# Kernel optimization log

Measured on AMD Instinct MI355X. Metric: run time of the kernel, lower is better.

The kernel has to match this reference:

```python
import jax, jax.numpy as jnp
import numpy as np

HEADS = 8
DIM_HEAD = 64
SCALE = DIM_HEAD ** -0.5
K = 7


def _conv(x, w, stride):
    return jax.lax.conv_general_dilated(
        x, w, window_strides=(stride, stride), padding='VALID',
        dimension_numbers=('NHWC', 'HWIO', 'NHWC'))


def _split_heads(t):
    # 'b x y (h d) -> (b h) (x y) d'
    b, X, Y, hd = t.shape
    d = hd // HEADS
    t = t.reshape(b, X, Y, HEADS, d)
    t = t.transpose(0, 3, 1, 2, 4)  # b h x y d
    return t.reshape(b * HEADS, X * Y, d)


def setup_inputs() -> dict:
    key = jax.random.key(0)
    ks = jax.random.split(key, 6)
    dim, inner = 256, HEADS * DIM_HEAD
    x = jax.random.normal(ks[0], (8, 84, 84, dim), dtype=jnp.float32)
    w_q = jax.random.normal(ks[1], (1, 1, dim, inner), dtype=jnp.float32) * 0.02
    w_kv = jax.random.normal(ks[2], (K, K, dim, 2 * inner), dtype=jnp.float32) * 0.02
    w_out = jax.random.normal(ks[3], (1, 1, inner, dim), dtype=jnp.float32) * 0.02
    b_out = jnp.zeros((dim,), dtype=jnp.float32)
    return {"x": x, "w_q": w_q, "w_kv": w_kv, "w_out": w_out, "b_out": b_out}


def reference(x, w_q, w_kv, w_out, b_out):
    b, X, Y, _ = x.shape
    q = _conv(x, w_q, 1)          # [b, X, Y, inner]
    kv = _conv(x, w_kv, K)        # [b, X/k, Y/k, 2*inner]
    k, v = jnp.split(kv, 2, axis=-1)
    q = _split_heads(q)           # [(b h), XY, d]
    k = _split_heads(k)           # [(b h), xy, d]
    v = _split_heads(v)
    dots = jnp.einsum('bid,bjd->bij', q, k) * SCALE
    attn = jax.nn.softmax(dots, axis=-1)
    out = jnp.einsum('bij,bjd->bid', attn, v)  # [(b h), XY, d]
    out = out.reshape(b, HEADS, X, Y, DIM_HEAD).transpose(0, 2, 3, 1, 4)
    out = out.reshape(b, X, Y, HEADS * DIM_HEAD)
    out = _conv(out, w_out, 1) + b_out  # dropout rate 0 -> identity
    return out
```

## Files before the change

### kernel.cpp

```cpp
#include <hip/hip_runtime.h>

typedef unsigned short u16;
typedef __bf16 bf16x8 __attribute__((ext_vector_type(8)));
typedef float f32x4 __attribute__((ext_vector_type(4)));

__device__ __forceinline__ u16 f2b(float f) {
    unsigned int u = __float_as_uint(f);
    u += 0x7fffu + ((u >> 16) & 1u);
    return (u16)(u >> 16);
}

__device__ __forceinline__ int xcd_chunk(int wg, int n) {
    int q = n >> 3, r = n & 7;
    int x = wg & 7, i = wg >> 3;
    return (x < r ? x * (q + 1) : r * (q + 1) + (x - r) * q) + i;
}

__global__ __launch_bounds__(256) void k_pack_x(const float* __restrict__ x,
                                                u16* __restrict__ xp) {
    int v = blockIdx.x * 256 + threadIdx.x;
    int c0 = (v & 31) << 3;
    int pix = v >> 5;
    int b = pix / 7056;
    int r = pix - b * 7056;
    int y = r / 84;
    int xx = r - y * 84;
    int opix = (b * 144 + (y / 7) * 12 + (xx / 7)) * 49 + (y % 7) * 7 + (xx % 7);
    const float4* src = reinterpret_cast<const float4*>(x + ((size_t)pix << 8) + c0);
    float4 f0 = src[0], f1 = src[1];
    uint4 o;
    o.x = (unsigned)f2b(f0.x) | ((unsigned)f2b(f0.y) << 16);
    o.y = (unsigned)f2b(f0.z) | ((unsigned)f2b(f0.w) << 16);
    o.z = (unsigned)f2b(f1.x) | ((unsigned)f2b(f1.y) << 16);
    o.w = (unsigned)f2b(f1.z) | ((unsigned)f2b(f1.w) << 16);
    *reinterpret_cast<uint4*>(xp + ((size_t)opix << 8) + c0) = o;
}

__global__ __launch_bounds__(256) void k_tconv(const float* __restrict__ in,
                                               u16* __restrict__ out, int R, int C,
                                               float scale) {
    __shared__ float tile[32][33];
    int c0 = blockIdx.x << 5, r0 = blockIdx.y << 5;
    int tx = threadIdx.x, ty = threadIdx.y;
#pragma unroll
    for (int i = 0; i < 4; i++)
        tile[ty + (i << 3)][tx] = in[(size_t)(r0 + ty + (i << 3)) * C + c0 + tx];
    __syncthreads();
#pragma unroll
    for (int i = 0; i < 4; i++)
        out[(size_t)(c0 + ty + (i << 3)) * R + r0 + tx] = f2b(tile[tx][ty + (i << 3)] * scale);
}

__global__ __launch_bounds__(256) void k_kvproj(const u16* __restrict__ xp,
                                                const u16* __restrict__ wkvT,
                                                float* __restrict__ parts) {
    __shared__ u16 As[128][72];
    __shared__ u16 Bs[128][72];
    const int lin = xcd_chunk(blockIdx.x, 504);
    const int mt = lin % 9;
    const int ntsp = lin / 9;
    const int nt = ntsp & 7;
    const int sp = ntsp >> 3;
    const int tid = threadIdx.x;
    const int wave = tid >> 6, lane = tid & 63;
    const int wr = wave >> 1, wc = wave & 1;
    const int lrow = lane & 15, lkg = lane >> 4;
    const u16* Ag = xp + (size_t)(mt * 128) * 12544 + sp * 1792;
    const u16* Bg = wkvT + (size_t)(nt * 128) * 12544 + sp * 1792;
    const int srow = tid >> 3, scol = (tid & 7) << 3;
    f32x4 acc[4][4];
#pragma unroll
    for (int m = 0; m < 4; m++)
#pragma unroll
        for (int n = 0; n < 4; n++)
#pragma unroll
            for (int i = 0; i < 4; i++) acc[m][n][i] = 0.f;

    for (int ks = 0; ks < 28; ks++) {
        const int k0 = ks * 64;
        __syncthreads();
#pragma unroll
        for (int p = 0; p < 4; p++) {
            int rr = srow + (p << 5);
            *reinterpret_cast<bf16x8*>(&As[rr][scol]) =
                *reinterpret_cast<const bf16x8*>(Ag + (size_t)rr * 12544 + k0 + scol);
            *reinterpret_cast<bf16x8*>(&Bs[rr][scol]) =
                *reinterpret_cast<const bf16x8*>(Bg + (size_t)rr * 12544 + k0 + scol);
        }
        __syncthreads();
#pragma unroll
        for (int kk = 0; kk < 2; kk++) {
            const int ko = (kk << 5) + (lkg << 3);
            bf16x8 a[4], bb[4];
#pragma unroll
            for (int m = 0; m < 4; m++)
                a[m] = *reinterpret_cast<const bf16x8*>(&As[(wr << 6) + (m << 4) + lrow][ko]);
#pragma unroll
            for (int n = 0; n < 4; n++)
                bb[n] = *reinterpret_cast<const bf16x8*>(&Bs[(wc << 6) + (n << 4) + lrow][ko]);
#pragma unroll
            for (int m = 0; m < 4; m++)
#pragma unroll
                for (int n = 0; n < 4; n++)
                    acc[m][n] = __builtin_amdgcn_mfma_f32_16x16x32_bf16(a[m], bb[n], acc[m][n], 0, 0, 0);
        }
    }
    float* outp = parts + (size_t)sp * 1179648;
#pragma unroll
    for (int m = 0; m < 4; m++)
#pragma unroll
        for (int n = 0; n < 4; n++)
#pragma unroll
            for (int i = 0; i < 4; i++) {
                int row = (mt << 7) + (wr << 6) + (m << 4) + (lkg << 2) + i;
                int col = (nt << 7) + (wc << 6) + (n << 4) + lrow;
                outp[(size_t)row * 1024 + col] = acc[m][n][i];
            }
}

__global__ __launch_bounds__(256) void k_kvfin(const float* __restrict__ parts,
                                               u16* __restrict__ Kf, u16* __restrict__ Vf) {
    int idx = blockIdx.x * 256 + threadIdx.x;
    int m = idx >> 10, n = idx & 1023;
    float s = 0.f;
#pragma unroll
    for (int sp = 0; sp < 7; sp++) s += parts[(size_t)sp * 1179648 + idx];
    int b = m / 144, pi = m - b * 144;
    int h = (n & 511) >> 6, d = n & 63;
    int bh = (b << 3) + h;
    if (n < 512) {
        int fc = pi >> 4, lr = pi & 15;
        int ks = d >> 5, lg = (d >> 3) & 3, e = d & 7;
        Kf[((((size_t)bh * 9 + fc) << 1) + ks) * 512 + (((lg << 4) + lr) << 3) + e] = f2b(s);
    } else {
        int nf = d >> 4, lr = d & 15;
        int ks = pi >> 5, lg = (pi >> 3) & 3, e = pi & 7;
        Vf[(((size_t)bh * 4 + nf) * 5 + ks) * 512 + (((lg << 4) + lr) << 3) + e] = f2b(s);
    }
}

__global__ __launch_bounds__(256) void k_qproj(const u16* __restrict__ xp,
                                               const u16* __restrict__ wqT,
                                               u16* __restrict__ Qf) {
    __shared__ u16 As[128][72];
    __shared__ u16 Bs[128][72];
    const int lin = xcd_chunk(blockIdx.x, 1764);
    const int nt = lin & 3, mt = lin >> 2;
    const int tid = threadIdx.x;
    const int wave = tid >> 6, lane = tid & 63;
    const int wr = wave >> 1, wc = wave & 1;
    const int lrow = lane & 15, lkg = lane >> 4;
    const u16* Ag = xp + (size_t)(mt * 128) * 256;
    const u16* Bg = wqT + (size_t)(nt * 128) * 256;
    const int srow = tid >> 3, scol = (tid & 7) << 3;
    f32x4 acc[4][4];
#pragma unroll
    for (int m = 0; m < 4; m++)
#pragma unroll
        for (int n = 0; n < 4; n++)
#pragma unroll
            for (int i = 0; i < 4; i++) acc[m][n][i] = 0.f;

    for (int ks = 0; ks < 4; ks++) {
        const int k0 = ks * 64;
        __syncthreads();
#pragma unroll
        for (int p = 0; p < 4; p++) {
            int rr = srow + (p << 5);
            *reinterpret_cast<bf16x8*>(&As[rr][scol]) =
                *reinterpret_cast<const bf16x8*>(Ag + (size_t)rr * 256 + k0 + scol);
            *reinterpret_cast<bf16x8*>(&Bs[rr][scol]) =
                *reinterpret_cast<const bf16x8*>(Bg + (size_t)rr * 256 + k0 + scol);
        }
        __syncthreads();
#pragma unroll
        for (int kk = 0; kk < 2; kk++) {
            const int ko = (kk << 5) + (lkg << 3);
            bf16x8 a[4], bb[4];
#pragma unroll
            for (int m = 0; m < 4; m++)
                a[m] = *reinterpret_cast<const bf16x8*>(&As[(wr << 6) + (m << 4) + lrow][ko]);
#pragma unroll
            for (int n = 0; n < 4; n++)
                bb[n] = *reinterpret_cast<const bf16x8*>(&Bs[(wc << 6) + (n << 4) + lrow][ko]);
#pragma unroll
            for (int m = 0; m < 4; m++)
#pragma unroll
                for (int n = 0; n < 4; n++)
                    acc[m][n] = __builtin_amdgcn_mfma_f32_16x16x32_bf16(a[m], bb[n], acc[m][n], 0, 0, 0);
        }
    }
#pragma unroll
    for (int m = 0; m < 4; m++)
#pragma unroll
        for (int n = 0; n < 4; n++)
#pragma unroll
            for (int i = 0; i < 4; i++) {
                int row = (mt << 7) + (wr << 6) + (m << 4) + (lkg << 2) + i;
                int col = (nt << 7) + (wc << 6) + (n << 4) + lrow;
                int b = row / 7056, pp = row - b * 7056;
                int h = col >> 6, d = col & 63;
                int bh = (b << 3) + h;
                int tt = pp >> 4, flr = pp & 15;
                int fks = d >> 5, flg = (d >> 3) & 3, fe = d & 7;
                Qf[((((size_t)bh * 441 + tt) << 1) + fks) * 512 + (((flg << 4) + flr) << 3) + fe] =
                    f2b(acc[m][n][i]);
            }
}

__global__ __launch_bounds__(128, 8) void k_attn(const u16* __restrict__ Qf,
                                                 const u16* __restrict__ Kf,
                                                 const u16* __restrict__ Vf,
                                                 u16* __restrict__ O) {
    __shared__ u16 smem[2 * 16 * 168];
    const int wv = threadIdx.x >> 6, lane = threadIdx.x & 63;
    const int t = blockIdx.x;
    const int h = (blockIdx.y << 1) + wv;
    const int b = blockIdx.z;
    const int lrow = lane & 15, lkg = lane >> 4;
    const int bh = (b << 3) + h;
    u16* sm = smem + wv * (16 * 168);
    const int l8 = lane << 3;

    const u16* Qg = Qf + ((((size_t)bh * 441 + t) << 1) << 9);
    const u16* Kg = Kf + (((size_t)bh * 9) << 10);
    const u16* Vg = Vf + ((size_t)bh * 20) * 512;

    f32x4 da[9];
#pragma unroll
    for (int fc = 0; fc < 9; fc++)
#pragma unroll
        for (int i = 0; i < 4; i++) da[fc][i] = 0.f;
#pragma unroll
    for (int ks = 0; ks < 2; ks++) {
        bf16x8 aq = *reinterpret_cast<const bf16x8*>(Qg + (ks << 9) + l8);
#pragma unroll
        for (int fc = 0; fc < 9; fc++) {
            bf16x8 bk = *reinterpret_cast<const bf16x8*>(Kg + ((((fc << 1) + ks)) << 9) + l8);
            da[fc] = __builtin_amdgcn_mfma_f32_16x16x32_bf16(aq, bk, da[fc], 0, 0, 0);
        }
    }

#pragma unroll
    for (int i = 0; i < 4; i++) {
        float mx = -1e30f;
#pragma unroll
        for (int fc = 0; fc < 9; fc++) mx = fmaxf(mx, da[fc][i]);
#pragma unroll
        for (int s = 1; s < 16; s <<= 1) mx = fmaxf(mx, __shfl_xor(mx, s));
        float e[9];
        float sum = 0.f;
#pragma unroll
        for (int fc = 0; fc < 9; fc++) {
            e[fc] = __expf(da[fc][i] - mx);
            sum += e[fc];
        }
#pragma unroll
        for (int s = 1; s < 16; s <<= 1) sum += __shfl_xor(sum, s);
        float inv = 1.0f / sum;
        int r = (lkg << 2) + i;
#pragma unroll
        for (int fc = 0; fc < 9; fc++) sm[r * 168 + (fc << 4) + lrow] = f2b(e[fc] * inv);
        sm[r * 168 + 144 + lrow] = 0;
    }
    asm volatile("" ::: "memory");

    f32x4 oa[4];
#pragma unroll
    for (int n = 0; n < 4; n++)
#pragma unroll
        for (int i = 0; i < 4; i++) oa[n][i] = 0.f;
#pragma unroll
    for (int ks = 0; ks < 5; ks++) {
        const int k0 = (ks << 5) + (lkg << 3);
        bf16x8 pa = *reinterpret_cast<const bf16x8*>(sm + (size_t)lrow * 168 + k0);
#pragma unroll
        for (int n = 0; n < 4; n++) {
            bf16x8 bv = *reinterpret_cast<const bf16x8*>(Vg + ((size_t)(n * 5 + ks) << 9) + l8);
            oa[n] = __builtin_amdgcn_mfma_f32_16x16x32_bf16(pa, bv, oa[n], 0, 0, 0);
        }
    }

#pragma unroll
    for (int n = 0; n < 4; n++)
#pragma unroll
        for (int i = 0; i < 4; i++) {
            int r = (lkg << 2) + i;
            int q = (t << 4) + r;
            int pi = q / 49, pos = q - pi * 49;
            int y = (pi / 12) * 7 + pos / 7;
            int xx = (pi - (pi / 12) * 12) * 7 + (pos - (pos / 7) * 7);
            O[(((size_t)b * 7056 + y * 84 + xx) << 9) + (h << 6) + (n << 4) + lrow] =
                f2b(oa[n][i]);
        }
}

__global__ __launch_bounds__(256) void k_outproj(const u16* __restrict__ A,
                                                 const u16* __restrict__ BT,
                                                 const float* __restrict__ bias,
                                                 float* __restrict__ out) {
    __shared__ u16 As[128][72];
    __shared__ u16 Bs[128][72];
    const int lin = xcd_chunk(blockIdx.x, 882);
    const int nt = lin & 1, mt = lin >> 1;
    const int tid = threadIdx.x;
    const int wave = tid >> 6, lane = tid & 63;
    const int wr = wave >> 1, wc = wave & 1;
    const int lrow = lane & 15, lkg = lane >> 4;
    const u16* Ag = A + (size_t)(mt * 128) * 512;
    const u16* Bg = BT + (size_t)(nt * 128) * 512;
    const int srow = tid >> 3, scol = (tid & 7) << 3;
    f32x4 acc[4][4];
#pragma unroll
    for (int m = 0; m < 4; m++)
#pragma unroll
        for (int n = 0; n < 4; n++)
#pragma unroll
            for (int i = 0; i < 4; i++) acc[m][n][i] = 0.f;

    for (int ks = 0; ks < 8; ks++) {
        const int k0 = ks * 64;
        __syncthreads();
#pragma unroll
        for (int p = 0; p < 4; p++) {
            int rr = srow + (p << 5);
            *reinterpret_cast<bf16x8*>(&As[rr][scol]) =
                *reinterpret_cast<const bf16x8*>(Ag + (size_t)rr * 512 + k0 + scol);
            *reinterpret_cast<bf16x8*>(&Bs[rr][scol]) =
                *reinterpret_cast<const bf16x8*>(Bg + (size_t)rr * 512 + k0 + scol);
        }
        __syncthreads();
#pragma unroll
        for (int kk = 0; kk < 2; kk++) {
            const int ko = (kk << 5) + (lkg << 3);
            bf16x8 a[4], bb[4];
#pragma unroll
            for (int m = 0; m < 4; m++)
                a[m] = *reinterpret_cast<const bf16x8*>(&As[(wr << 6) + (m << 4) + lrow][ko]);
#pragma unroll
            for (int n = 0; n < 4; n++)
                bb[n] = *reinterpret_cast<const bf16x8*>(&Bs[(wc << 6) + (n << 4) + lrow][ko]);
#pragma unroll
            for (int m = 0; m < 4; m++)
#pragma unroll
                for (int n = 0; n < 4; n++)
                    acc[m][n] = __builtin_amdgcn_mfma_f32_16x16x32_bf16(a[m], bb[n], acc[m][n], 0, 0, 0);
        }
    }
#pragma unroll
    for (int m = 0; m < 4; m++)
#pragma unroll
        for (int n = 0; n < 4; n++)
#pragma unroll
            for (int i = 0; i < 4; i++) {
                int row = (mt << 7) + (wr << 6) + (m << 4) + (lkg << 2) + i;
                int col = (nt << 7) + (wc << 6) + (n << 4) + lrow;
                out[(size_t)row * 256 + col] = acc[m][n][i] + bias[col];
            }
}

extern "C" void kernel_launch(void* const* d_in, const int* in_sizes, int n_in,
                              void* d_out, int out_size, void* d_ws, size_t ws_size,
                              hipStream_t stream) {
    const float* x = (const float*)d_in[0];
    const float* w_q = (const float*)d_in[1];
    const float* w_kv = (const float*)d_in[2];
    const float* w_out = (const float*)d_in[3];
    const float* b_out = (const float*)d_in[4];
    float* out = (float*)d_out;

    char* ws = (char*)d_ws;
    size_t off = 0;
    auto alloc = [&](size_t bytes) -> char* {
        char* p = ws + off;
        off = (off + bytes + 255) & ~(size_t)255;
        return p;
    };
    u16* xp = (u16*)alloc(28901376ull);
    u16* wqT = (u16*)alloc(262144ull);
    u16* woutT = (u16*)alloc(262144ull);
    u16* Kf = (u16*)alloc(1179648ull);
    u16* Vf = (u16*)alloc(1310720ull);
    u16* O = (u16*)alloc(57802752ull);
    u16* wkvT = (u16*)alloc(25690112ull);
    float* parts = (float*)alloc(33030144ull);
    u16* Qf = (u16*)wkvT;

    hipMemsetAsync(Vf, 0, 1310720ull, stream);
    k_pack_x<<<7056, 256, 0, stream>>>(x, xp);
    k_tconv<<<dim3(32, 392), dim3(32, 8), 0, stream>>>(w_kv, wkvT, 12544, 1024, 1.0f);
    k_tconv<<<dim3(16, 8), dim3(32, 8), 0, stream>>>(w_q, wqT, 256, 512, 0.125f);
    k_tconv<<<dim3(8, 16), dim3(32, 8), 0, stream>>>(w_out, woutT, 512, 256, 1.0f);
    k_kvproj<<<504, 256, 0, stream>>>(xp, wkvT, parts);
    k_kvfin<<<4608, 256, 0, stream>>>(parts, Kf, Vf);
    k_qproj<<<1764, 256, 0, stream>>>(xp, wqT, Qf);
    k_attn<<<dim3(441, 4, 8), 128, 0, stream>>>(Qf, Kf, Vf, O);
    k_outproj<<<882, 256, 0, stream>>>(O, woutT, b_out, out);
}
```

Measured before the change: 226.7 us.

## Use direct global-to-LDS loads in kvproj, vectorize attention output stores, native bf16 converts

The kvproj GEMM now stages its A and B tiles with global_load_lds instead of loading through registers into padded shared arrays. This drops the row padding, so the LDS fragment reads may hit more bank conflicts. The attention epilogue writes four bf16 values per lane in one vector store. To keep the outproj GEMM correct, the w_out transpose permutes its K index to match the new column order of the attention output. The float-to-bf16 conversion now uses the native __bf16 cast, both in the x packing and elsewhere.

```diff
diff --git a/kernel.cpp b/kernel.cpp
--- a/kernel.cpp
+++ b/kernel.cpp
@@ -2,12 +2,12 @@
 
 typedef unsigned short u16;
 typedef __bf16 bf16x8 __attribute__((ext_vector_type(8)));
+typedef __bf16 bf16x4 __attribute__((ext_vector_type(4)));
 typedef float f32x4 __attribute__((ext_vector_type(4)));
 
 __device__ __forceinline__ u16 f2b(float f) {
-    unsigned int u = __float_as_uint(f);
-    u += 0x7fffu + ((u >> 16) & 1u);
-    return (u16)(u >> 16);
+    __bf16 h = (__bf16)f;
+    return __builtin_bit_cast(u16, h);
 }
 
 __device__ __forceinline__ int xcd_chunk(int wg, int n) {
@@ -15,6 +15,11 @@
     int x = wg & 7, i = wg >> 3;
     return (x < r ? x * (q + 1) : r * (q + 1) + (x - r) * q) + i;
 }
+
+#define GLOAD_LDS16(src, dst)                                              \
+    __builtin_amdgcn_global_load_lds(                                      \
+        (const __attribute__((address_space(1))) void*)(src),              \
+        (__attribute__((address_space(3))) void*)(dst), 16, 0, 0)
 
 __global__ __launch_bounds__(256) void k_pack_x(const float* __restrict__ x,
                                                 u16* __restrict__ xp) {
@@ -28,17 +33,14 @@
     int opix = (b * 144 + (y / 7) * 12 + (xx / 7)) * 49 + (y % 7) * 7 + (xx % 7);
     const float4* src = reinterpret_cast<const float4*>(x + ((size_t)pix << 8) + c0);
     float4 f0 = src[0], f1 = src[1];
-    uint4 o;
-    o.x = (unsigned)f2b(f0.x) | ((unsigned)f2b(f0.y) << 16);
-    o.y = (unsigned)f2b(f0.z) | ((unsigned)f2b(f0.w) << 16);
-    o.z = (unsigned)f2b(f1.x) | ((unsigned)f2b(f1.y) << 16);
-    o.w = (unsigned)f2b(f1.z) | ((unsigned)f2b(f1.w) << 16);
-    *reinterpret_cast<uint4*>(xp + ((size_t)opix << 8) + c0) = o;
+    bf16x8 o = {(__bf16)f0.x, (__bf16)f0.y, (__bf16)f0.z, (__bf16)f0.w,
+                (__bf16)f1.x, (__bf16)f1.y, (__bf16)f1.z, (__bf16)f1.w};
+    *reinterpret_cast<bf16x8*>(xp + ((size_t)opix << 8) + c0) = o;
 }
 
 __global__ __launch_bounds__(256) void k_tconv(const float* __restrict__ in,
                                                u16* __restrict__ out, int R, int C,
-                                               float scale) {
+                                               float scale, int permk) {
     __shared__ float tile[32][33];
     int c0 = blockIdx.x << 5, r0 = blockIdx.y << 5;
     int tx = threadIdx.x, ty = threadIdx.y;
@@ -46,16 +48,18 @@
     for (int i = 0; i < 4; i++)
         tile[ty + (i << 3)][tx] = in[(size_t)(r0 + ty + (i << 3)) * C + c0 + tx];
     __syncthreads();
+    int k = r0 + tx;
+    int kw = permk ? ((k & ~63) | ((k & 15) << 2) | ((k >> 4) & 3)) : k;
 #pragma unroll
     for (int i = 0; i < 4; i++)
-        out[(size_t)(c0 + ty + (i << 3)) * R + r0 + tx] = f2b(tile[tx][ty + (i << 3)] * scale);
+        out[(size_t)(c0 + ty + (i << 3)) * R + kw] = f2b(tile[tx][ty + (i << 3)] * scale);
 }
 
 __global__ __launch_bounds__(256) void k_kvproj(const u16* __restrict__ xp,
                                                 const u16* __restrict__ wkvT,
                                                 float* __restrict__ parts) {
-    __shared__ u16 As[128][72];
-    __shared__ u16 Bs[128][72];
+    __shared__ u16 As[8192];
+    __shared__ u16 Bs[8192];
     const int lin = xcd_chunk(blockIdx.x, 504);
     const int mt = lin % 9;
     const int ntsp = lin / 9;
@@ -67,7 +71,7 @@
     const int lrow = lane & 15, lkg = lane >> 4;
     const u16* Ag = xp + (size_t)(mt * 128) * 12544 + sp * 1792;
     const u16* Bg = wkvT + (size_t)(nt * 128) * 12544 + sp * 1792;
-    const int srow = tid >> 3, scol = (tid & 7) << 3;
+    const int srow = lane >> 3, scol = (lane & 7) << 3;
     f32x4 acc[4][4];
 #pragma unroll
     for (int m = 0; m < 4; m++)
@@ -77,15 +81,14 @@
             for (int i = 0; i < 4; i++) acc[m][n][i] = 0.f;
 
     for (int ks = 0; ks < 28; ks++) {
-        const int k0 = ks * 64;
-        __syncthreads();
-#pragma unroll
-        for (int p = 0; p < 4; p++) {
-            int rr = srow + (p << 5);
-            *reinterpret_cast<bf16x8*>(&As[rr][scol]) =
-                *reinterpret_cast<const bf16x8*>(Ag + (size_t)rr * 12544 + k0 + scol);
-            *reinterpret_cast<bf16x8*>(&Bs[rr][scol]) =
-                *reinterpret_cast<const bf16x8*>(Bg + (size_t)rr * 12544 + k0 + scol);
+        const int k0 = ks << 6;
+        __syncthreads();
+#pragma unroll
+        for (int j = 0; j < 4; j++) {
+            const int c = (wave << 2) + j;
+            const int row = (c << 3) + srow;
+            GLOAD_LDS16(Ag + (size_t)row * 12544 + k0 + scol, As + (c << 9));
+            GLOAD_LDS16(Bg + (size_t)row * 12544 + k0 + scol, Bs + (c << 9));
         }
         __syncthreads();
 #pragma unroll
@@ -94,10 +97,10 @@
             bf16x8 a[4], bb[4];
 #pragma unroll
             for (int m = 0; m < 4; m++)
-                a[m] = *reinterpret_cast<const bf16x8*>(&As[(wr << 6) + (m << 4) + lrow][ko]);
+                a[m] = *reinterpret_cast<const bf16x8*>(As + (((wr << 6) + (m << 4) + lrow) << 6) + ko);
 #pragma unroll
             for (int n = 0; n < 4; n++)
-                bb[n] = *reinterpret_cast<const bf16x8*>(&Bs[(wc << 6) + (n << 4) + lrow][ko]);
+                bb[n] = *reinterpret_cast<const bf16x8*>(Bs + (((wc << 6) + (n << 4) + lrow) << 6) + ko);
 #pragma unroll
             for (int m = 0; m < 4; m++)
 #pragma unroll
@@ -282,17 +285,16 @@
     }
 
 #pragma unroll
-    for (int n = 0; n < 4; n++)
-#pragma unroll
-        for (int i = 0; i < 4; i++) {
-            int r = (lkg << 2) + i;
-            int q = (t << 4) + r;
-            int pi = q / 49, pos = q - pi * 49;
-            int y = (pi / 12) * 7 + pos / 7;
-            int xx = (pi - (pi / 12) * 12) * 7 + (pos - (pos / 7) * 7);
-            O[(((size_t)b * 7056 + y * 84 + xx) << 9) + (h << 6) + (n << 4) + lrow] =
-                f2b(oa[n][i]);
-        }
+    for (int i = 0; i < 4; i++) {
+        int r = (lkg << 2) + i;
+        int q = (t << 4) + r;
+        int pi = q / 49, pos = q - pi * 49;
+        int y = (pi / 12) * 7 + pos / 7;
+        int xx = (pi - (pi / 12) * 12) * 7 + (pos - (pos / 7) * 7);
+        bf16x4 ov = {(__bf16)oa[0][i], (__bf16)oa[1][i], (__bf16)oa[2][i], (__bf16)oa[3][i]};
+        *reinterpret_cast<bf16x4*>(O + (((size_t)b * 7056 + y * 84 + xx) << 9) +
+                                   (h << 6) + (lrow << 2)) = ov;
+    }
 }
 
 __global__ __launch_bounds__(256) void k_outproj(const u16* __restrict__ A,
@@ -388,9 +390,9 @@
 
     hipMemsetAsync(Vf, 0, 1310720ull, stream);
     k_pack_x<<<7056, 256, 0, stream>>>(x, xp);
-    k_tconv<<<dim3(32, 392), dim3(32, 8), 0, stream>>>(w_kv, wkvT, 12544, 1024, 1.0f);
-    k_tconv<<<dim3(16, 8), dim3(32, 8), 0, stream>>>(w_q, wqT, 256, 512, 0.125f);
-    k_tconv<<<dim3(8, 16), dim3(32, 8), 0, stream>>>(w_out, woutT, 512, 256, 1.0f);
+    k_tconv<<<dim3(32, 392), dim3(32, 8), 0, stream>>>(w_kv, wkvT, 12544, 1024, 1.0f, 0);
+    k_tconv<<<dim3(16, 8), dim3(32, 8), 0, stream>>>(w_q, wqT, 256, 512, 0.125f, 0);
+    k_tconv<<<dim3(8, 16), dim3(32, 8), 0, stream>>>(w_out, woutT, 512, 256, 1.0f, 1);
     k_kvproj<<<504, 256, 0, stream>>>(xp, wkvT, parts);
     k_kvfin<<<4608, 256, 0, stream>>>(parts, Kf, Vf);
     k_qproj<<<1764, 256, 0, stream>>>(xp, wqT, Qf);
```

After: 229.9 us. No clear change (+1.4%).
